# Kernel tuning notes

Hardware: AMD Instinct MI355X
Metric: run time of the kernel (lower is better)

The kernel has to match this reference:

```python
import jax, jax.numpy as jnp
import numpy as np

N = 200000   # nodes
E = 6400000  # directed edges (avg degree 32)
F = 128      # num_features
C = 16       # num_classes
H1, H2, H3 = 4, 4, 2  # hardcoded GCN hidden dims from the source


def setup_inputs():
    key = jax.random.key(0)
    ks = jax.random.split(key, 10)
    x = jax.random.normal(ks[0], (N, F), dtype=jnp.float32)
    edge_index = jax.random.randint(ks[1], (2, E), 0, N, dtype=jnp.int32)
    def lin(k, fin, fout):
        return jax.random.normal(k, (fin, fout), dtype=jnp.float32) / np.sqrt(fin).astype(np.float32)
    return {
        "x": x,
        "W1": lin(ks[2], F, H1),  "b1": jnp.zeros((H1,), jnp.float32),
        "W2": lin(ks[3], H1, H2), "b2": jnp.zeros((H2,), jnp.float32),
        "W3": lin(ks[4], H2, H3), "b3": jnp.zeros((H3,), jnp.float32),
        "Wc": lin(ks[5], H3, C),  "bc": jnp.zeros((C,), jnp.float32),
        "edge_index": edge_index,
    }


def _gcn_conv(h, W, b, src, dst, norm, n):
    # PyG GCNConv: linear first, then normalized scatter-add aggregation, then bias
    h = h @ W                                   # [n, fout]
    msg = h[src] * norm[:, None]                # gather + per-edge scale
    out = jax.ops.segment_sum(msg, dst, num_segments=n)
    return out + b


def reference(x, W1, b1, W2, b2, W3, b3, Wc, bc, edge_index):
    n = x.shape[0]
    # add self-loops (GCNConv default add_self_loops=True)
    loop = jnp.arange(n, dtype=edge_index.dtype)
    src = jnp.concatenate([edge_index[0], loop])
    dst = jnp.concatenate([edge_index[1], loop])
    # symmetric degree normalization: norm_e = deg(dst)^-1/2 * deg(src)^-1/2
    deg = jax.ops.segment_sum(jnp.ones(src.shape[0], dtype=x.dtype), dst, num_segments=n)
    dinv = jnp.where(deg > 0, jax.lax.rsqrt(deg), jnp.zeros_like(deg))
    norm = dinv[src] * dinv[dst]
    h = jnp.tanh(_gcn_conv(x, W1, b1, src, dst, norm, n))
    h = jnp.tanh(_gcn_conv(h, W2, b2, src, dst, norm, n))
    h = jnp.tanh(_gcn_conv(h, W3, b3, src, dst, norm, n))
    out = h @ Wc + bc
    return (out, h)
```

## Files before the change

kernel.cpp:

```cpp
#include <hip/hip_runtime.h>
#include <math.h>


#define NR 1000
#define RNG 200
#define CAP 8192
#define HB 1024
#define EPT 8
#define EPB (HB * EPT)
#define SCAP 8192
#define Q 8
#define LROWS 32
#define LPAD 133


__global__ void k_initcur(int* __restrict__ cursor) {
    int t = blockIdx.x * blockDim.x + threadIdx.x;
    if (t < NR) cursor[t * 16] = t * CAP;
}

__global__ __launch_bounds__(HB) void k_build(const int* __restrict__ src,
                                              const int* __restrict__ dst,
                                              int* __restrict__ cursor,
                                              int* __restrict__ csrp, int e) {
    __shared__ int hist[NR];
    __shared__ int scn[HB];
    __shared__ int start[NR + 1];
    __shared__ int gbase[NR];
    __shared__ int cur[NR];
    __shared__ int buf[EPB];

    int t = threadIdx.x;
    for (int i = t; i < NR; i += HB) hist[i] = 0;
    __syncthreads();

    int ds[EPT], sr[EPT];
    int base = blockIdx.x * EPB;
#pragma unroll
    for (int k = 0; k < 2; k++) {
        int idx = base + k * HB * 4 + t * 4;
        if (idx + 3 < e) {
            int4 d4 = *(const int4*)(dst + idx);
            int4 s4 = *(const int4*)(src + idx);
            ds[4 * k + 0] = d4.x; ds[4 * k + 1] = d4.y; ds[4 * k + 2] = d4.z; ds[4 * k + 3] = d4.w;
            sr[4 * k + 0] = s4.x; sr[4 * k + 1] = s4.y; sr[4 * k + 2] = s4.z; sr[4 * k + 3] = s4.w;
        } else {
#pragma unroll
            for (int j = 0; j < 4; j++) {
                int i2 = idx + j;
                if (i2 < e) { ds[4 * k + j] = dst[i2]; sr[4 * k + j] = src[i2]; }
                else ds[4 * k + j] = -1;
            }
        }
    }
#pragma unroll
    for (int k = 0; k < EPT; k++)
        if (ds[k] >= 0) atomicAdd(&hist[ds[k] / RNG], 1);
    __syncthreads();

    scn[t] = (t < NR) ? hist[t] : 0;
    __syncthreads();
    for (int off = 1; off < HB; off <<= 1) {
        int add = (t >= off) ? scn[t - off] : 0;
        __syncthreads();
        scn[t] += add;
        __syncthreads();
    }
    if (t < NR) {
        int c = hist[t];
        int st = scn[t] - c;
        start[t] = st;
        cur[t] = st;
        gbase[t] = c ? atomicAdd(&cursor[t * 16], c) : 0;
    }
    if (t == 0) start[NR] = scn[NR - 1];
    __syncthreads();

#pragma unroll
    for (int k = 0; k < EPT; k++) {
        if (ds[k] >= 0) {
            int bin = ds[k] / RNG;
            int p = atomicAdd(&cur[bin], 1);
            buf[p] = (sr[k] << 8) | (ds[k] - bin * RNG);
        }
    }
    __syncthreads();

    int total = start[NR];
    for (int j = t; j < total; j += HB) {
        int lo = 0, hi = NR;
        while (hi - lo > 1) {
            int mid = (lo + hi) >> 1;
            if (start[mid] <= j) lo = mid; else hi = mid;
        }
        int g = gbase[lo] + (j - start[lo]);
        if (g < (lo + 1) * CAP) csrp[g] = buf[j];
    }
}


__global__ __launch_bounds__(1024) void k_sortbin(int* __restrict__ csrp,
                                                  const int* __restrict__ cursor,
                                                  float* __restrict__ dinv, int n) {
    __shared__ int deg[RNG];
    __shared__ int off[RNG];
    __shared__ int cur[RNG];
    __shared__ int sbuf[SCAP];
    int t = threadIdx.x, b = blockIdx.x;
    int s0 = b * CAP;
    int cnt = cursor[b * 16] - s0;
    if (cnt < 0) cnt = 0; if (cnt > CAP) cnt = CAP;

    for (int i = t; i < RNG; i += 1024) deg[i] = 0;
    __syncthreads();
    for (int j = t; j < cnt; j += 1024)
        atomicAdd(&deg[csrp[s0 + j] & 255], 1);
    __syncthreads();

    if (t < RNG) off[t] = deg[t];
    __syncthreads();
    for (int d = 1; d < RNG; d <<= 1) {
        int u = 0;
        if (t < RNG && t >= d) u = off[t - d];
        __syncthreads();
        if (t < RNG) off[t] += u;
        __syncthreads();
    }
    if (t < RNG) cur[t] = off[t] - deg[t];
    __syncthreads();

    for (int j = t; j < cnt; j += 1024) {
        int p = csrp[s0 + j];
        int r = atomicAdd(&cur[p & 255], 1);
        if (r < SCAP) sbuf[r] = p;
    }
    __syncthreads();
    int lim = (cnt < SCAP) ? cnt : SCAP;
    for (int j = t; j < lim; j += 1024)
        csrp[s0 + j] = sbuf[j];

    int basen = b * RNG;
    for (int i = t; i < RNG; i += 1024) {
        int node = basen + i;
        if (node < n) dinv[node] = rsqrtf(1.0f + (float)deg[i]);
    }
}


__global__ __launch_bounds__(256) void k_linear1(const float* __restrict__ x,
                                                 const float* __restrict__ W1,
                                                 const float* __restrict__ dinv,
                                                 float4* __restrict__ g1, int n) {
    __shared__ float xs[LROWS * LPAD];
    int t = threadIdx.x;
    int q = t & 7, r = t >> 3;
    int row0 = blockIdx.x * LROWS;

    float4 w[16];
#pragma unroll
    for (int i = 0; i < 16; i++) w[i] = ((const float4*)W1)[q * 16 + i];

    const float4* xg = (const float4*)(x + (size_t)row0 * 128);
    int maxI = (n - row0) * 32;
#pragma unroll
    for (int k = 0; k < 4; k++) {
        int idx = t + k * 256;
        if (idx < maxI) {
            float4 v = xg[idx];
            int rr = idx >> 5, cc = (idx & 31) << 2;
            *(float4*)&xs[rr * LPAD + cc] = v;
        }
    }
    __syncthreads();

    float p0 = 0.f, p1 = 0.f, p2 = 0.f, p3 = 0.f;
    const float* xr = &xs[r * LPAD + q * 16];
#pragma unroll
    for (int j = 0; j < 4; j++) {
        float4 xv = *(const float4*)(xr + 4 * j);
        float4 wa = w[4 * j + 0], wb = w[4 * j + 1], wc = w[4 * j + 2], wd = w[4 * j + 3];
        p0 += xv.x * wa.x + xv.y * wb.x + xv.z * wc.x + xv.w * wd.x;
        p1 += xv.x * wa.y + xv.y * wb.y + xv.z * wc.y + xv.w * wd.y;
        p2 += xv.x * wa.z + xv.y * wb.z + xv.z * wc.z + xv.w * wd.z;
        p3 += xv.x * wa.w + xv.y * wb.w + xv.z * wc.w + xv.w * wd.w;
    }
#pragma unroll
    for (int off = 1; off < 8; off <<= 1) {
        p0 += __shfl_xor(p0, off, 64);
        p1 += __shfl_xor(p1, off, 64);
        p2 += __shfl_xor(p2, off, 64);
        p3 += __shfl_xor(p3, off, 64);
    }
    int row = row0 + r;
    if (q == 0 && row < n) {
        float dv = dinv[row];
        g1[row] = make_float4(dv * p0, dv * p1, dv * p2, dv * p3);
    }
}


#define PUSH4() { qd[qc * 256 + t] = cd; \
    qv[(qc * 4 + 0) * 256 + t] = a0; qv[(qc * 4 + 1) * 256 + t] = a1; \
    qv[(qc * 4 + 2) * 256 + t] = a2; qv[(qc * 4 + 3) * 256 + t] = a3; qc++; }
#define EDGE4(di, gv) { int d_ = (di) & 255; \
    if (d_ != cd) { if (cd >= 0) PUSH4(); cd = d_; a0 = gv.x; a1 = gv.y; a2 = gv.z; a3 = gv.w; } \
    else { a0 += gv.x; a1 += gv.y; a2 += gv.z; a3 += gv.w; } }
#define FLUSH4() { for (int q = 0; q < Q; q++) { if (q < qc) { int dd = qd[q * 256 + t]; \
    atomicAdd(&acc[dd * 5 + 0], qv[(q * 4 + 0) * 256 + t]); \
    atomicAdd(&acc[dd * 5 + 1], qv[(q * 4 + 1) * 256 + t]); \
    atomicAdd(&acc[dd * 5 + 2], qv[(q * 4 + 2) * 256 + t]); \
    atomicAdd(&acc[dd * 5 + 3], qv[(q * 4 + 3) * 256 + t]); } } qc = 0; }

#define EDGELOOP4P() \
    int s0 = b * CAP; \
    int cnt = cursor[b * 16] - s0; if (cnt < 0) cnt = 0; if (cnt > CAP) cnt = CAP; \
    int per = (((cnt + 255) >> 8) + 3) & ~3; \
    int lo = s0 + t * per; \
    int hi = lo + per; int eE = s0 + cnt; if (hi > eE) hi = eE; \
    int cd = -1; float a0 = 0, a1 = 0, a2 = 0, a3 = 0; \
    int qc = 0; \
    int4 pA, pB; \
    float4 gA0, gA1, gA2, gA3; \
    if (lo < hi) { \
        pA = *(const int4*)(csrp + lo); \
        int mA = hi - lo; \
        int e1 = (mA > 1) ? pA.y : pA.x; \
        int e2 = (mA > 2) ? pA.z : pA.x; \
        int e3 = (mA > 3) ? pA.w : pA.x; \
        gA0 = gin[(unsigned)pA.x >> 8]; gA1 = gin[(unsigned)e1 >> 8]; \
        gA2 = gin[(unsigned)e2 >> 8]; gA3 = gin[(unsigned)e3 >> 8]; \
        int jB = lo + 4; \
        pB = *(const int4*)(csrp + ((jB < hi) ? jB : lo)); \
    } \
    for (int j = lo; j < hi; j += 4) { \
        int4 p = pA; \
        float4 g0 = gA0, g1 = gA1, g2 = gA2, g3 = gA3; \
        int m = hi - j; \
        int jn = j + 4; \
        pA = pB; \
        if (jn < hi) { \
            int mN = hi - jn; \
            int e1 = (mN > 1) ? pA.y : pA.x; \
            int e2 = (mN > 2) ? pA.z : pA.x; \
            int e3 = (mN > 3) ? pA.w : pA.x; \
            gA0 = gin[(unsigned)pA.x >> 8]; gA1 = gin[(unsigned)e1 >> 8]; \
            gA2 = gin[(unsigned)e2 >> 8]; gA3 = gin[(unsigned)e3 >> 8]; \
        } \
        int jB2 = j + 8; \
        pB = *(const int4*)(csrp + ((jB2 < hi) ? jB2 : lo)); \
        int i1 = (m > 1) ? p.y : p.x; \
        int i2 = (m > 2) ? p.z : p.x; \
        int i3 = (m > 3) ? p.w : p.x; \
        EDGE4(p.x, g0); \
        if (m > 1) EDGE4(i1, g1); \
        if (m > 2) EDGE4(i2, g2); \
        if (m > 3) EDGE4(i3, g3); \
        if (__any(qc >= Q - 3)) FLUSH4(); \
    } \
    if (cd >= 0) PUSH4(); \
    FLUSH4(); \
    __syncthreads();

__global__ __launch_bounds__(256) void k_bagg44s(const int* __restrict__ csrp,
                                                 const int* __restrict__ cursor,
                                                 const float* __restrict__ dinv,
                                                 const float4* __restrict__ gin,
                                                 float4* __restrict__ gout,
                                                 const float* __restrict__ W,
                                                 const float* __restrict__ bv, int n) {
    __shared__ float acc[RNG * 5];
    __shared__ float qv[Q * 4 * 256];
    __shared__ int   qd[Q * 256];
    int t = threadIdx.x, b = blockIdx.x;
    for (int i = t; i < RNG * 5; i += 256) acc[i] = 0.0f;
    __syncthreads();
    EDGELOOP4P();
    int basen = b * RNG;
    for (int i = t; i < RNG; i += 256) {
        int node = basen + i;
        if (node >= n) continue;
        float4 gs = gin[node];
        float dv = dinv[node];
        float t0 = tanhf(dv * (gs.x + acc[i * 5 + 0]) + bv[0]);
        float t1 = tanhf(dv * (gs.y + acc[i * 5 + 1]) + bv[1]);
        float t2 = tanhf(dv * (gs.z + acc[i * 5 + 2]) + bv[2]);
        float t3 = tanhf(dv * (gs.w + acc[i * 5 + 3]) + bv[3]);
        float4 o;
        o.x = dv * (t0 * W[0] + t1 * W[4] + t2 * W[8]  + t3 * W[12]);
        o.y = dv * (t0 * W[1] + t1 * W[5] + t2 * W[9]  + t3 * W[13]);
        o.z = dv * (t0 * W[2] + t1 * W[6] + t2 * W[10] + t3 * W[14]);
        o.w = dv * (t0 * W[3] + t1 * W[7] + t2 * W[11] + t3 * W[15]);
        gout[node] = o;
    }
}

__global__ __launch_bounds__(256) void k_bagg42s(const int* __restrict__ csrp,
                                                 const int* __restrict__ cursor,
                                                 const float* __restrict__ dinv,
                                                 const float4* __restrict__ gin,
                                                 float2* __restrict__ gout,
                                                 const float* __restrict__ W,
                                                 const float* __restrict__ bv, int n) {
    __shared__ float acc[RNG * 5];
    __shared__ float qv[Q * 4 * 256];
    __shared__ int   qd[Q * 256];
    int t = threadIdx.x, b = blockIdx.x;
    for (int i = t; i < RNG * 5; i += 256) acc[i] = 0.0f;
    __syncthreads();
    EDGELOOP4P();
    int basen = b * RNG;
    for (int i = t; i < RNG; i += 256) {
        int node = basen + i;
        if (node >= n) continue;
        float4 gs = gin[node];
        float dv = dinv[node];
        float t0 = tanhf(dv * (gs.x + acc[i * 5 + 0]) + bv[0]);
        float t1 = tanhf(dv * (gs.y + acc[i * 5 + 1]) + bv[1]);
        float t2 = tanhf(dv * (gs.z + acc[i * 5 + 2]) + bv[2]);
        float t3 = tanhf(dv * (gs.w + acc[i * 5 + 3]) + bv[3]);
        float h0 = t0 * W[0] + t1 * W[2] + t2 * W[4] + t3 * W[6];
        float h1 = t0 * W[1] + t1 * W[3] + t2 * W[5] + t3 * W[7];
        gout[node] = make_float2(dv * h0, dv * h1);
    }
}

#define PUSH2() { qd[qc * 256 + t] = cd; \
    qv[(qc * 2 + 0) * 256 + t] = a0; qv[(qc * 2 + 1) * 256 + t] = a1; qc++; }
#define EDGE2(di, gv) { int d_ = (di) & 255; \
    if (d_ != cd) { if (cd >= 0) PUSH2(); cd = d_; a0 = gv.x; a1 = gv.y; } \
    else { a0 += gv.x; a1 += gv.y; } }
#define FLUSH2() { for (int q = 0; q < Q; q++) { if (q < qc) { int dd = qd[q * 256 + t]; \
    atomicAdd(&acc[dd * 3 + 0], qv[(q * 2 + 0) * 256 + t]); \
    atomicAdd(&acc[dd * 3 + 1], qv[(q * 2 + 1) * 256 + t]); } } qc = 0; }

__global__ __launch_bounds__(256) void k_bagg2outs(const int* __restrict__ csrp,
                                                   const int* __restrict__ cursor,
                                                   const float* __restrict__ dinv,
                                                   const float2* __restrict__ gin,
                                                   const float* __restrict__ b3,
                                                   const float* __restrict__ Wc,
                                                   const float* __restrict__ bc,
                                                   float* __restrict__ out,
                                                   float2* __restrict__ hout, int n) {
    __shared__ float acc[RNG * 3];
    __shared__ float qv[Q * 2 * 256];
    __shared__ int   qd[Q * 256];
    int t = threadIdx.x, b = blockIdx.x;
    for (int i = t; i < RNG * 3; i += 256) acc[i] = 0.0f;
    __syncthreads();
    int s0 = b * CAP;
    int cnt = cursor[b * 16] - s0; if (cnt < 0) cnt = 0; if (cnt > CAP) cnt = CAP;
    int per = (((cnt + 255) >> 8) + 3) & ~3;
    int lo = s0 + t * per;
    int hi = lo + per; int eE = s0 + cnt; if (hi > eE) hi = eE;
    int cd = -1; float a0 = 0, a1 = 0;
    int qc = 0;
    int4 pA, pB;
    float2 gA0, gA1, gA2, gA3;
    if (lo < hi) {
        pA = *(const int4*)(csrp + lo);
        int mA = hi - lo;
        int e1 = (mA > 1) ? pA.y : pA.x;
        int e2 = (mA > 2) ? pA.z : pA.x;
        int e3 = (mA > 3) ? pA.w : pA.x;
        gA0 = gin[(unsigned)pA.x >> 8]; gA1 = gin[(unsigned)e1 >> 8];
        gA2 = gin[(unsigned)e2 >> 8]; gA3 = gin[(unsigned)e3 >> 8];
        int jB = lo + 4;
        pB = *(const int4*)(csrp + ((jB < hi) ? jB : lo));
    }
    for (int j = lo; j < hi; j += 4) {
        int4 p = pA;
        float2 g0 = gA0, g1 = gA1, g2 = gA2, g3 = gA3;
        int m = hi - j;
        int jn = j + 4;
        pA = pB;
        if (jn < hi) {
            int mN = hi - jn;
            int e1 = (mN > 1) ? pA.y : pA.x;
            int e2 = (mN > 2) ? pA.z : pA.x;
            int e3 = (mN > 3) ? pA.w : pA.x;
            gA0 = gin[(unsigned)pA.x >> 8]; gA1 = gin[(unsigned)e1 >> 8];
            gA2 = gin[(unsigned)e2 >> 8]; gA3 = gin[(unsigned)e3 >> 8];
        }
        int jB2 = j + 8;
        pB = *(const int4*)(csrp + ((jB2 < hi) ? jB2 : lo));
        int i1 = (m > 1) ? p.y : p.x;
        int i2 = (m > 2) ? p.z : p.x;
        int i3 = (m > 3) ? p.w : p.x;
        EDGE2(p.x, g0);
        if (m > 1) EDGE2(i1, g1);
        if (m > 2) EDGE2(i2, g2);
        if (m > 3) EDGE2(i3, g3);
        if (__any(qc >= Q - 3)) FLUSH2();
    }
    if (cd >= 0) PUSH2();
    FLUSH2();
    __syncthreads();
    int basen = b * RNG;
    for (int i = t; i < RNG; i += 256) {
        int node = basen + i;
        if (node >= n) continue;
        float2 gs = gin[node];
        float dv = dinv[node];
        float t0 = tanhf(dv * (gs.x + acc[i * 3 + 0]) + b3[0]);
        float t1 = tanhf(dv * (gs.y + acc[i * 3 + 1]) + b3[1]);
        hout[node] = make_float2(t0, t1);
        float4* o = (float4*)(out + (size_t)node * 16);
#pragma unroll
        for (int q = 0; q < 4; q++) {
            float4 v;
            v.x = t0 * Wc[4 * q + 0] + t1 * Wc[16 + 4 * q + 0] + bc[4 * q + 0];
            v.y = t0 * Wc[4 * q + 1] + t1 * Wc[16 + 4 * q + 1] + bc[4 * q + 1];
            v.z = t0 * Wc[4 * q + 2] + t1 * Wc[16 + 4 * q + 2] + bc[4 * q + 2];
            v.w = t0 * Wc[4 * q + 3] + t1 * Wc[16 + 4 * q + 3] + bc[4 * q + 3];
            o[q] = v;
        }
    }
}


__global__ void k_count(const int* __restrict__ dst, int* __restrict__ cnt, int e) {
    int i = blockIdx.x * blockDim.x + threadIdx.x;
    if (i < e) atomicAdd(&cnt[dst[i]], 1);
}

__global__ void k_dinv_i(const int* __restrict__ cnt, float* __restrict__ dinv, int n) {
    int i = blockIdx.x * blockDim.x + threadIdx.x;
    if (i < n) dinv[i] = rsqrtf(1.0f + (float)cnt[i]);
}

__global__ void f_linear1(const float* __restrict__ x, const float* __restrict__ W1,
                          const float* __restrict__ dinv,
                          float* __restrict__ h, float* __restrict__ agg, int n) {
    int lane = threadIdx.x & 63;
    int wave = blockIdx.x * (blockDim.x >> 6) + (threadIdx.x >> 6);
    int nwaves = gridDim.x * (blockDim.x >> 6);
    float4 w0 = ((const float4*)W1)[2 * lane];
    float4 w1 = ((const float4*)W1)[2 * lane + 1];
    for (int row = wave; row < n; row += nwaves) {
        float2 xv = ((const float2*)(x + (size_t)row * 128))[lane];
        float p0 = xv.x * w0.x + xv.y * w1.x;
        float p1 = xv.x * w0.y + xv.y * w1.y;
        float p2 = xv.x * w0.z + xv.y * w1.z;
        float p3 = xv.x * w0.w + xv.y * w1.w;
#pragma unroll
        for (int off = 32; off; off >>= 1) {
            p0 += __shfl_xor(p0, off, 64);
            p1 += __shfl_xor(p1, off, 64);
            p2 += __shfl_xor(p2, off, 64);
            p3 += __shfl_xor(p3, off, 64);
        }
        if (lane == 0) {
            float dv = dinv[row]; float dv2 = dv * dv;
            ((float4*)h)[row] = make_float4(p0, p1, p2, p3);
            ((float4*)agg)[row] = make_float4(dv2 * p0, dv2 * p1, dv2 * p2, dv2 * p3);
        }
    }
}

__global__ void k_edge4(const int* __restrict__ src, const int* __restrict__ dst,
                        const float* __restrict__ dinv, const float* __restrict__ h,
                        float* __restrict__ agg, int e) {
    int i = blockIdx.x * blockDim.x + threadIdx.x;
    if (i >= e) return;
    int s = src[i], d = dst[i];
    float w = dinv[s] * dinv[d];
    float4 hv = ((const float4*)h)[s];
    float* a = agg + 4 * (size_t)d;
    unsafeAtomicAdd(a + 0, w * hv.x);
    unsafeAtomicAdd(a + 1, w * hv.y);
    unsafeAtomicAdd(a + 2, w * hv.z);
    unsafeAtomicAdd(a + 3, w * hv.w);
}

__global__ void k_edge2(const int* __restrict__ src, const int* __restrict__ dst,
                        const float* __restrict__ dinv, const float* __restrict__ h,
                        float* __restrict__ agg, int e) {
    int i = blockIdx.x * blockDim.x + threadIdx.x;
    if (i >= e) return;
    int s = src[i], d = dst[i];
    float w = dinv[s] * dinv[d];
    float2 hv = ((const float2*)h)[s];
    float* a = agg + 2 * (size_t)d;
    unsafeAtomicAdd(a + 0, w * hv.x);
    unsafeAtomicAdd(a + 1, w * hv.y);
}

__global__ void k_fin44(float* __restrict__ h, float* __restrict__ agg,
                        const float* __restrict__ dinv,
                        const float* __restrict__ W, const float* __restrict__ b, int n) {
    int i = blockIdx.x * blockDim.x + threadIdx.x;
    if (i >= n) return;
    float4 a = ((const float4*)agg)[i];
    float t0 = tanhf(a.x + b[0]);
    float t1 = tanhf(a.y + b[1]);
    float t2 = tanhf(a.z + b[2]);
    float t3 = tanhf(a.w + b[3]);
    float hn[4];
#pragma unroll
    for (int k = 0; k < 4; k++)
        hn[k] = t0 * W[k] + t1 * W[4 + k] + t2 * W[8 + k] + t3 * W[12 + k];
    float dv = dinv[i], dv2 = dv * dv;
    ((float4*)h)[i] = make_float4(hn[0], hn[1], hn[2], hn[3]);
    ((float4*)agg)[i] = make_float4(dv2 * hn[0], dv2 * hn[1], dv2 * hn[2], dv2 * hn[3]);
}

__global__ void k_fin42(const float* __restrict__ agg, float* __restrict__ h3,
                        float* __restrict__ agg3, const float* __restrict__ dinv,
                        const float* __restrict__ W, const float* __restrict__ b, int n) {
    int i = blockIdx.x * blockDim.x + threadIdx.x;
    if (i >= n) return;
    float4 a = ((const float4*)agg)[i];
    float t0 = tanhf(a.x + b[0]);
    float t1 = tanhf(a.y + b[1]);
    float t2 = tanhf(a.z + b[2]);
    float t3 = tanhf(a.w + b[3]);
    float h0 = t0 * W[0] + t1 * W[2] + t2 * W[4] + t3 * W[6];
    float h1 = t0 * W[1] + t1 * W[3] + t2 * W[5] + t3 * W[7];
    float dv = dinv[i], dv2 = dv * dv;
    ((float2*)h3)[i] = make_float2(h0, h1);
    ((float2*)agg3)[i] = make_float2(dv2 * h0, dv2 * h1);
}

__global__ void k_final_old(const float* __restrict__ agg3,
                            const float* __restrict__ Wc, const float* __restrict__ b3,
                            const float* __restrict__ bc,
                            float* __restrict__ out, float* __restrict__ hout, int n) {
    int i = blockIdx.x * blockDim.x + threadIdx.x;
    if (i >= n) return;
    float2 a = ((const float2*)agg3)[i];
    float t0 = tanhf(a.x + b3[0]);
    float t1 = tanhf(a.y + b3[1]);
    ((float2*)hout)[i] = make_float2(t0, t1);
    float4* o = (float4*)(out + (size_t)i * 16);
#pragma unroll
    for (int q = 0; q < 4; q++) {
        float4 v;
        v.x = t0 * Wc[4 * q + 0] + t1 * Wc[16 + 4 * q + 0] + bc[4 * q + 0];
        v.y = t0 * Wc[4 * q + 1] + t1 * Wc[16 + 4 * q + 1] + bc[4 * q + 1];
        v.z = t0 * Wc[4 * q + 2] + t1 * Wc[16 + 4 * q + 2] + bc[4 * q + 2];
        v.w = t0 * Wc[4 * q + 3] + t1 * Wc[16 + 4 * q + 3] + bc[4 * q + 3];
        o[q] = v;
    }
}


extern "C" void kernel_launch(void* const* d_in, const int* in_sizes, int n_in,
                              void* d_out, int out_size, void* d_ws, size_t ws_size,
                              hipStream_t stream) {
    const float* x   = (const float*)d_in[0];
    const float* W1  = (const float*)d_in[1];
    const float* b1  = (const float*)d_in[2];
    const float* W2  = (const float*)d_in[3];
    const float* b2  = (const float*)d_in[4];
    const float* W3  = (const float*)d_in[5];
    const float* b3  = (const float*)d_in[6];
    const float* Wc  = (const float*)d_in[7];
    const float* bc  = (const float*)d_in[8];
    const int* eidx  = (const int*)d_in[9];

    const int n = in_sizes[0] / 128;
    const int e = in_sizes[9] / 2;
    const int* src = eidx;
    const int* dst = eidx + e;

    float* out_c = (float*)d_out;
    float* out_h = (float*)d_out + 16 * (size_t)n;

    const int B = 256;
    const int gn = (n + B - 1) / B;
    const int ge = (e + B - 1) / B;
    const int nbE = (e + EPB - 1) / EPB;

    size_t nP = ((size_t)n + 3) & ~(size_t)3;

    int* csrp    = (int*)d_ws;
    int* cursor  = csrp + (size_t)NR * CAP + 4096;
    float* dinv  = (float*)(cursor + NR * 16);
    float* g1    = dinv + nP;
    float* g2    = g1 + 4 * nP;
    float* g3    = g2 + 4 * nP;
    size_t need  = (size_t)((char*)(g3 + 2 * nP) - (char*)d_ws);

    bool fast = (ws_size >= need) && (n <= NR * RNG) && (n < (1 << 18));

    if (fast) {
        k_initcur<<<(NR + 255) / 256, 256, 0, stream>>>(cursor);
        k_build<<<nbE, HB, 0, stream>>>(src, dst, cursor, csrp, e);
        k_sortbin<<<NR, 1024, 0, stream>>>(csrp, cursor, dinv, n);

        k_linear1<<<(n + LROWS - 1) / LROWS, 256, 0, stream>>>(x, W1, dinv, (float4*)g1, n);
        k_bagg44s<<<NR, 256, 0, stream>>>(csrp, cursor, dinv, (const float4*)g1,
                                          (float4*)g2, W2, b1, n);
        k_bagg42s<<<NR, 256, 0, stream>>>(csrp, cursor, dinv, (const float4*)g2,
                                          (float2*)g3, W3, b2, n);
        k_bagg2outs<<<NR, 256, 0, stream>>>(csrp, cursor, dinv, (const float2*)g3,
                                            b3, Wc, bc, out_c, (float2*)out_h, n);
    } else {
        int* fcnt   = (int*)d_ws;
        float* fdnv = (float*)d_ws + nP;
        float* h    = fdnv + nP;
        float* agg  = h + 4 * nP;
        float* h3   = agg + 4 * nP;
        float* agg3 = h3 + 2 * nP;

        hipMemsetAsync(fcnt, 0, (size_t)n * sizeof(int), stream);
        k_count<<<ge, B, 0, stream>>>(dst, fcnt, e);
        k_dinv_i<<<gn, B, 0, stream>>>(fcnt, fdnv, n);
        f_linear1<<<(n + 3) / 4, B, 0, stream>>>(x, W1, fdnv, h, agg, n);
        k_edge4<<<ge, B, 0, stream>>>(src, dst, fdnv, h, agg, e);
        k_fin44<<<gn, B, 0, stream>>>(h, agg, fdnv, W2, b1, n);
        k_edge4<<<ge, B, 0, stream>>>(src, dst, fdnv, h, agg, e);
        k_fin42<<<gn, B, 0, stream>>>(agg, h3, agg3, fdnv, W3, b2, n);
        k_edge2<<<ge, B, 0, stream>>>(src, dst, fdnv, h3, agg3, e);
        k_final_old<<<gn, B, 0, stream>>>(agg3, Wc, b3, bc, out_c, (float*)out_h, n);
    }
}
```

Baseline: 422.7 us.

## Use wider bins split into quarter-blocks with padded segments, drop LDS flush queues

The bins become 400 nodes wide (500 bins with larger capacity), and each bin is split into four 100-node quarters. Each quarter's edge segment is padded to a multiple of 4 with dummy entries that point to a zeroed sentinel row, so the aggregation loops can drop their tail masking. The aggregation kernels launch four blocks per bin and accumulate straight into a small LDS array with atomics, replacing the per-thread queue-and-flush buffers. k_build now stores the bin id per edge instead of binary-searching for it. The changes aim to raise occupancy and cut LDS use and branching, at the cost of more LDS atomic contention and larger sort buffers.

Result: faster. 376.3 us (-11.0%).

```diff
diff --git a/kernel.cpp b/kernel.cpp
--- a/kernel.cpp
+++ b/kernel.cpp
@@ -2,22 +2,27 @@
 #include <math.h>
 
 
-#define NR 1000
-#define RNG 200
-#define CAP 8192
+#define NR 500
+#define RNG 400
+#define CAP 16384
 #define HB 1024
 #define EPT 8
 #define EPB (HB * EPT)
-#define SCAP 8192
-#define Q 8
+#define SCAP 14348
+#define QBLK 100
 #define LROWS 32
 #define LPAD 133
 
 
-__global__ void k_initcur(int* __restrict__ cursor) {
+__global__ void k_initcur(int* __restrict__ cursor, float* __restrict__ g1,
+                          float* __restrict__ g2, float* __restrict__ g3, int n) {
     int t = blockIdx.x * blockDim.x + threadIdx.x;
     if (t < NR) cursor[t * 16] = t * CAP;
-}
+    if (t < 4) g1[4 * (size_t)n + t] = 0.0f;
+    if (t >= 4 && t < 8) g2[4 * (size_t)n + (t - 4)] = 0.0f;
+    if (t >= 8 && t < 10) g3[2 * (size_t)n + (t - 8)] = 0.0f;
+}
+
 
 __global__ __launch_bounds__(HB) void k_build(const int* __restrict__ src,
                                               const int* __restrict__ dst,
@@ -29,6 +34,7 @@
     __shared__ int gbase[NR];
     __shared__ int cur[NR];
     __shared__ int buf[EPB];
+    __shared__ short bbin[EPB];
 
     int t = threadIdx.x;
     for (int i = t; i < NR; i += HB) hist[i] = 0;
@@ -81,30 +87,29 @@
         if (ds[k] >= 0) {
             int bin = ds[k] / RNG;
             int p = atomicAdd(&cur[bin], 1);
-            buf[p] = (sr[k] << 8) | (ds[k] - bin * RNG);
+            buf[p] = (sr[k] << 9) | (ds[k] - bin * RNG);
+            bbin[p] = (short)bin;
         }
     }
     __syncthreads();
 
     int total = start[NR];
     for (int j = t; j < total; j += HB) {
-        int lo = 0, hi = NR;
-        while (hi - lo > 1) {
-            int mid = (lo + hi) >> 1;
-            if (start[mid] <= j) lo = mid; else hi = mid;
-        }
-        int g = gbase[lo] + (j - start[lo]);
-        if (g < (lo + 1) * CAP) csrp[g] = buf[j];
+        int bin = bbin[j];
+        int g = gbase[bin] + (j - start[bin]);
+        if (g < (bin + 1) * CAP) csrp[g] = buf[j];
     }
 }
 
 
 __global__ __launch_bounds__(1024) void k_sortbin(int* __restrict__ csrp,
                                                   const int* __restrict__ cursor,
+                                                  int* __restrict__ split,
                                                   float* __restrict__ dinv, int n) {
     __shared__ int deg[RNG];
     __shared__ int off[RNG];
     __shared__ int cur[RNG];
+    __shared__ int qb[5];
     __shared__ int sbuf[SCAP];
     int t = threadIdx.x, b = blockIdx.x;
     int s0 = b * CAP;
@@ -114,7 +119,7 @@
     for (int i = t; i < RNG; i += 1024) deg[i] = 0;
     __syncthreads();
     for (int j = t; j < cnt; j += 1024)
-        atomicAdd(&deg[csrp[s0 + j] & 255], 1);
+        atomicAdd(&deg[csrp[s0 + j] & 511], 1);
     __syncthreads();
 
     if (t < RNG) off[t] = deg[t];
@@ -126,16 +131,45 @@
         if (t < RNG) off[t] += u;
         __syncthreads();
     }
-    if (t < RNG) cur[t] = off[t] - deg[t];
+    __syncthreads();
+
+    if (t == 0) {
+        int e0 = off[99], e1 = off[199], e2 = off[299], e3 = off[399];
+        int b1 = (e0 + 3) & ~3;
+        int b2 = (b1 + (e1 - e0) + 3) & ~3;
+        int b3 = (b2 + (e2 - e1) + 3) & ~3;
+        int b4 = (b3 + (e3 - e2) + 3) & ~3;
+        qb[0] = 0; qb[1] = b1; qb[2] = b2; qb[3] = b3; qb[4] = b4;
+        split[b * 4 + 0] = b1; split[b * 4 + 1] = b2;
+        split[b * 4 + 2] = b3; split[b * 4 + 3] = b4;
+    }
+    __syncthreads();
+
+    if (t < RNG) {
+        int q = t / 100;
+        int bstart = (q == 0) ? 0 : off[q * 100 - 1];
+        cur[t] = (off[t] - deg[t]) - bstart + qb[q];
+    }
     __syncthreads();
 
     for (int j = t; j < cnt; j += 1024) {
         int p = csrp[s0 + j];
-        int r = atomicAdd(&cur[p & 255], 1);
+        int r = atomicAdd(&cur[p & 511], 1);
         if (r < SCAP) sbuf[r] = p;
     }
     __syncthreads();
-    int lim = (cnt < SCAP) ? cnt : SCAP;
+
+    if (t < 12) {
+        int q = t / 3, sl = t - q * 3;
+        int eq = off[q * 100 + 99];
+        int sq = (q == 0) ? 0 : off[q * 100 - 1];
+        int realend = qb[q] + (eq - sq);
+        int pos = realend + sl;
+        if (pos < qb[q + 1] && pos < SCAP) sbuf[pos] = (n << 9) | (q * 100);
+    }
+    __syncthreads();
+
+    int lim = qb[4]; if (lim > SCAP) lim = SCAP;
     for (int j = t; j < lim; j += 1024)
         csrp[s0 + j] = sbuf[j];
 
@@ -199,84 +233,65 @@
 }
 
 
-#define PUSH4() { qd[qc * 256 + t] = cd; \
-    qv[(qc * 4 + 0) * 256 + t] = a0; qv[(qc * 4 + 1) * 256 + t] = a1; \
-    qv[(qc * 4 + 2) * 256 + t] = a2; qv[(qc * 4 + 3) * 256 + t] = a3; qc++; }
-#define EDGE4(di, gv) { int d_ = (di) & 255; \
+#define PUSH4() { atomicAdd(&acc[cd * 5 + 0], a0); atomicAdd(&acc[cd * 5 + 1], a1); \
+    atomicAdd(&acc[cd * 5 + 2], a2); atomicAdd(&acc[cd * 5 + 3], a3); }
+#define EDGE4(di, gv) { int d_ = ((di) & 511) - qoff; \
     if (d_ != cd) { if (cd >= 0) PUSH4(); cd = d_; a0 = gv.x; a1 = gv.y; a2 = gv.z; a3 = gv.w; } \
     else { a0 += gv.x; a1 += gv.y; a2 += gv.z; a3 += gv.w; } }
-#define FLUSH4() { for (int q = 0; q < Q; q++) { if (q < qc) { int dd = qd[q * 256 + t]; \
-    atomicAdd(&acc[dd * 5 + 0], qv[(q * 4 + 0) * 256 + t]); \
-    atomicAdd(&acc[dd * 5 + 1], qv[(q * 4 + 1) * 256 + t]); \
-    atomicAdd(&acc[dd * 5 + 2], qv[(q * 4 + 2) * 256 + t]); \
-    atomicAdd(&acc[dd * 5 + 3], qv[(q * 4 + 3) * 256 + t]); } } qc = 0; }
 
 #define EDGELOOP4P() \
-    int s0 = b * CAP; \
-    int cnt = cursor[b * 16] - s0; if (cnt < 0) cnt = 0; if (cnt > CAP) cnt = CAP; \
-    int per = (((cnt + 255) >> 8) + 3) & ~3; \
-    int lo = s0 + t * per; \
-    int hi = lo + per; int eE = s0 + cnt; if (hi > eE) hi = eE; \
+    int bin = b >> 2, qq = b & 3; \
+    int qoff = qq * 100; \
+    int s0 = bin * CAP; \
+    int lo0 = qq ? split[bin * 4 + qq - 1] : 0; \
+    int hi0 = split[bin * 4 + qq]; \
+    int L = hi0 - lo0; \
+    int per = (((L + 255) >> 8) + 3) & ~3; \
+    int lo = s0 + lo0 + t * per; \
+    int hi = lo + per; int eE = s0 + hi0; if (hi > eE) hi = eE; \
     int cd = -1; float a0 = 0, a1 = 0, a2 = 0, a3 = 0; \
-    int qc = 0; \
     int4 pA, pB; \
     float4 gA0, gA1, gA2, gA3; \
     if (lo < hi) { \
         pA = *(const int4*)(csrp + lo); \
-        int mA = hi - lo; \
-        int e1 = (mA > 1) ? pA.y : pA.x; \
-        int e2 = (mA > 2) ? pA.z : pA.x; \
-        int e3 = (mA > 3) ? pA.w : pA.x; \
-        gA0 = gin[(unsigned)pA.x >> 8]; gA1 = gin[(unsigned)e1 >> 8]; \
-        gA2 = gin[(unsigned)e2 >> 8]; gA3 = gin[(unsigned)e3 >> 8]; \
+        gA0 = gin[(unsigned)pA.x >> 9]; gA1 = gin[(unsigned)pA.y >> 9]; \
+        gA2 = gin[(unsigned)pA.z >> 9]; gA3 = gin[(unsigned)pA.w >> 9]; \
         int jB = lo + 4; \
         pB = *(const int4*)(csrp + ((jB < hi) ? jB : lo)); \
     } \
     for (int j = lo; j < hi; j += 4) { \
         int4 p = pA; \
-        float4 g0 = gA0, g1 = gA1, g2 = gA2, g3 = gA3; \
-        int m = hi - j; \
+        float4 g0 = gA0, g1v = gA1, g2v = gA2, g3v = gA3; \
         int jn = j + 4; \
         pA = pB; \
         if (jn < hi) { \
-            int mN = hi - jn; \
-            int e1 = (mN > 1) ? pA.y : pA.x; \
-            int e2 = (mN > 2) ? pA.z : pA.x; \
-            int e3 = (mN > 3) ? pA.w : pA.x; \
-            gA0 = gin[(unsigned)pA.x >> 8]; gA1 = gin[(unsigned)e1 >> 8]; \
-            gA2 = gin[(unsigned)e2 >> 8]; gA3 = gin[(unsigned)e3 >> 8]; \
+            gA0 = gin[(unsigned)pA.x >> 9]; gA1 = gin[(unsigned)pA.y >> 9]; \
+            gA2 = gin[(unsigned)pA.z >> 9]; gA3 = gin[(unsigned)pA.w >> 9]; \
         } \
         int jB2 = j + 8; \
         pB = *(const int4*)(csrp + ((jB2 < hi) ? jB2 : lo)); \
-        int i1 = (m > 1) ? p.y : p.x; \
-        int i2 = (m > 2) ? p.z : p.x; \
-        int i3 = (m > 3) ? p.w : p.x; \
         EDGE4(p.x, g0); \
-        if (m > 1) EDGE4(i1, g1); \
-        if (m > 2) EDGE4(i2, g2); \
-        if (m > 3) EDGE4(i3, g3); \
-        if (__any(qc >= Q - 3)) FLUSH4(); \
+        EDGE4(p.y, g1v); \
+        EDGE4(p.z, g2v); \
+        EDGE4(p.w, g3v); \
     } \
     if (cd >= 0) PUSH4(); \
-    FLUSH4(); \
     __syncthreads();
 
 __global__ __launch_bounds__(256) void k_bagg44s(const int* __restrict__ csrp,
-                                                 const int* __restrict__ cursor,
+                                                 const int* __restrict__ split,
                                                  const float* __restrict__ dinv,
                                                  const float4* __restrict__ gin,
                                                  float4* __restrict__ gout,
                                                  const float* __restrict__ W,
                                                  const float* __restrict__ bv, int n) {
-    __shared__ float acc[RNG * 5];
-    __shared__ float qv[Q * 4 * 256];
-    __shared__ int   qd[Q * 256];
+    __shared__ float acc[QBLK * 5];
     int t = threadIdx.x, b = blockIdx.x;
-    for (int i = t; i < RNG * 5; i += 256) acc[i] = 0.0f;
+    for (int i = t; i < QBLK * 5; i += 256) acc[i] = 0.0f;
     __syncthreads();
     EDGELOOP4P();
-    int basen = b * RNG;
-    for (int i = t; i < RNG; i += 256) {
+    int basen = (b >> 2) * RNG + qoff;
+    for (int i = t; i < QBLK; i += 256) {
         int node = basen + i;
         if (node >= n) continue;
         float4 gs = gin[node];
@@ -295,21 +310,19 @@
 }
 
 __global__ __launch_bounds__(256) void k_bagg42s(const int* __restrict__ csrp,
-                                                 const int* __restrict__ cursor,
+                                                 const int* __restrict__ split,
                                                  const float* __restrict__ dinv,
                                                  const float4* __restrict__ gin,
                                                  float2* __restrict__ gout,
                                                  const float* __restrict__ W,
                                                  const float* __restrict__ bv, int n) {
-    __shared__ float acc[RNG * 5];
-    __shared__ float qv[Q * 4 * 256];
-    __shared__ int   qd[Q * 256];
+    __shared__ float acc[QBLK * 5];
     int t = threadIdx.x, b = blockIdx.x;
-    for (int i = t; i < RNG * 5; i += 256) acc[i] = 0.0f;
+    for (int i = t; i < QBLK * 5; i += 256) acc[i] = 0.0f;
     __syncthreads();
     EDGELOOP4P();
-    int basen = b * RNG;
-    for (int i = t; i < RNG; i += 256) {
+    int basen = (b >> 2) * RNG + qoff;
+    for (int i = t; i < QBLK; i += 256) {
         int node = basen + i;
         if (node >= n) continue;
         float4 gs = gin[node];
@@ -324,17 +337,13 @@
     }
 }
 
-#define PUSH2() { qd[qc * 256 + t] = cd; \
-    qv[(qc * 2 + 0) * 256 + t] = a0; qv[(qc * 2 + 1) * 256 + t] = a1; qc++; }
-#define EDGE2(di, gv) { int d_ = (di) & 255; \
+#define PUSH2() { atomicAdd(&acc[cd * 3 + 0], a0); atomicAdd(&acc[cd * 3 + 1], a1); }
+#define EDGE2(di, gv) { int d_ = ((di) & 511) - qoff; \
     if (d_ != cd) { if (cd >= 0) PUSH2(); cd = d_; a0 = gv.x; a1 = gv.y; } \
     else { a0 += gv.x; a1 += gv.y; } }
-#define FLUSH2() { for (int q = 0; q < Q; q++) { if (q < qc) { int dd = qd[q * 256 + t]; \
-    atomicAdd(&acc[dd * 3 + 0], qv[(q * 2 + 0) * 256 + t]); \
-    atomicAdd(&acc[dd * 3 + 1], qv[(q * 2 + 1) * 256 + t]); } } qc = 0; }
 
 __global__ __launch_bounds__(256) void k_bagg2outs(const int* __restrict__ csrp,
-                                                   const int* __restrict__ cursor,
+                                                   const int* __restrict__ split,
                                                    const float* __restrict__ dinv,
                                                    const float2* __restrict__ gin,
                                                    const float* __restrict__ b3,
@@ -342,62 +351,49 @@
                                                    const float* __restrict__ bc,
                                                    float* __restrict__ out,
                                                    float2* __restrict__ hout, int n) {
-    __shared__ float acc[RNG * 3];
-    __shared__ float qv[Q * 2 * 256];
-    __shared__ int   qd[Q * 256];
+    __shared__ float acc[QBLK * 3];
     int t = threadIdx.x, b = blockIdx.x;
-    for (int i = t; i < RNG * 3; i += 256) acc[i] = 0.0f;
-    __syncthreads();
-    int s0 = b * CAP;
-    int cnt = cursor[b * 16] - s0; if (cnt < 0) cnt = 0; if (cnt > CAP) cnt = CAP;
-    int per = (((cnt + 255) >> 8) + 3) & ~3;
-    int lo = s0 + t * per;
-    int hi = lo + per; int eE = s0 + cnt; if (hi > eE) hi = eE;
+    for (int i = t; i < QBLK * 3; i += 256) acc[i] = 0.0f;
+    __syncthreads();
+    int bin = b >> 2, qq = b & 3;
+    int qoff = qq * 100;
+    int s0 = bin * CAP;
+    int lo0 = qq ? split[bin * 4 + qq - 1] : 0;
+    int hi0 = split[bin * 4 + qq];
+    int L = hi0 - lo0;
+    int per = (((L + 255) >> 8) + 3) & ~3;
+    int lo = s0 + lo0 + t * per;
+    int hi = lo + per; int eE = s0 + hi0; if (hi > eE) hi = eE;
     int cd = -1; float a0 = 0, a1 = 0;
-    int qc = 0;
     int4 pA, pB;
     float2 gA0, gA1, gA2, gA3;
     if (lo < hi) {
         pA = *(const int4*)(csrp + lo);
-        int mA = hi - lo;
-        int e1 = (mA > 1) ? pA.y : pA.x;
-        int e2 = (mA > 2) ? pA.z : pA.x;
-        int e3 = (mA > 3) ? pA.w : pA.x;
-        gA0 = gin[(unsigned)pA.x >> 8]; gA1 = gin[(unsigned)e1 >> 8];
-        gA2 = gin[(unsigned)e2 >> 8]; gA3 = gin[(unsigned)e3 >> 8];
+        gA0 = gin[(unsigned)pA.x >> 9]; gA1 = gin[(unsigned)pA.y >> 9];
+        gA2 = gin[(unsigned)pA.z >> 9]; gA3 = gin[(unsigned)pA.w >> 9];
         int jB = lo + 4;
         pB = *(const int4*)(csrp + ((jB < hi) ? jB : lo));
     }
     for (int j = lo; j < hi; j += 4) {
         int4 p = pA;
-        float2 g0 = gA0, g1 = gA1, g2 = gA2, g3 = gA3;
-        int m = hi - j;
+        float2 g0 = gA0, g1v = gA1, g2v = gA2, g3v = gA3;
         int jn = j + 4;
         pA = pB;
         if (jn < hi) {
-            int mN = hi - jn;
-            int e1 = (mN > 1) ? pA.y : pA.x;
-            int e2 = (mN > 2) ? pA.z : pA.x;
-            int e3 = (mN > 3) ? pA.w : pA.x;
-            gA0 = gin[(unsigned)pA.x >> 8]; gA1 = gin[(unsigned)e1 >> 8];
-            gA2 = gin[(unsigned)e2 >> 8]; gA3 = gin[(unsigned)e3 >> 8];
+            gA0 = gin[(unsigned)pA.x >> 9]; gA1 = gin[(unsigned)pA.y >> 9];
+            gA2 = gin[(unsigned)pA.z >> 9]; gA3 = gin[(unsigned)pA.w >> 9];
         }
         int jB2 = j + 8;
         pB = *(const int4*)(csrp + ((jB2 < hi) ? jB2 : lo));
-        int i1 = (m > 1) ? p.y : p.x;
-        int i2 = (m > 2) ? p.z : p.x;
-        int i3 = (m > 3) ? p.w : p.x;
         EDGE2(p.x, g0);
-        if (m > 1) EDGE2(i1, g1);
-        if (m > 2) EDGE2(i2, g2);
-        if (m > 3) EDGE2(i3, g3);
-        if (__any(qc >= Q - 3)) FLUSH2();
+        EDGE2(p.y, g1v);
+        EDGE2(p.z, g2v);
+        EDGE2(p.w, g3v);
     }
     if (cd >= 0) PUSH2();
-    FLUSH2();
-    __syncthreads();
-    int basen = b * RNG;
-    for (int i = t; i < RNG; i += 256) {
+    __syncthreads();
+    int basen = bin * RNG + qoff;
+    for (int i = t; i < QBLK; i += 256) {
         int node = basen + i;
         if (node >= n) continue;
         float2 gs = gin[node];
@@ -572,11 +568,12 @@
     const int ge = (e + B - 1) / B;
     const int nbE = (e + EPB - 1) / EPB;
 
-    size_t nP = ((size_t)n + 3) & ~(size_t)3;
+    size_t nP = ((size_t)(n + 4) + 3) & ~(size_t)3;
 
     int* csrp    = (int*)d_ws;
     int* cursor  = csrp + (size_t)NR * CAP + 4096;
-    float* dinv  = (float*)(cursor + NR * 16);
+    int* split   = cursor + NR * 16;
+    float* dinv  = (float*)(split + NR * 4);
     float* g1    = dinv + nP;
     float* g2    = g1 + 4 * nP;
     float* g3    = g2 + 4 * nP;
@@ -585,17 +582,17 @@
     bool fast = (ws_size >= need) && (n <= NR * RNG) && (n < (1 << 18));
 
     if (fast) {
-        k_initcur<<<(NR + 255) / 256, 256, 0, stream>>>(cursor);
+        k_initcur<<<(NR + 255) / 256, 256, 0, stream>>>(cursor, g1, g2, g3, n);
         k_build<<<nbE, HB, 0, stream>>>(src, dst, cursor, csrp, e);
-        k_sortbin<<<NR, 1024, 0, stream>>>(csrp, cursor, dinv, n);
+        k_sortbin<<<NR, 1024, 0, stream>>>(csrp, cursor, split, dinv, n);
 
         k_linear1<<<(n + LROWS - 1) / LROWS, 256, 0, stream>>>(x, W1, dinv, (float4*)g1, n);
-        k_bagg44s<<<NR, 256, 0, stream>>>(csrp, cursor, dinv, (const float4*)g1,
-                                          (float4*)g2, W2, b1, n);
-        k_bagg42s<<<NR, 256, 0, stream>>>(csrp, cursor, dinv, (const float4*)g2,
-                                          (float2*)g3, W3, b2, n);
-        k_bagg2outs<<<NR, 256, 0, stream>>>(csrp, cursor, dinv, (const float2*)g3,
-                                            b3, Wc, bc, out_c, (float2*)out_h, n);
+        k_bagg44s<<<NR * 4, 256, 0, stream>>>(csrp, split, dinv, (const float4*)g1,
+                                              (float4*)g2, W2, b1, n);
+        k_bagg42s<<<NR * 4, 256, 0, stream>>>(csrp, split, dinv, (const float4*)g2,
+                                              (float2*)g3, W3, b2, n);
+        k_bagg2outs<<<NR * 4, 256, 0, stream>>>(csrp, split, dinv, (const float2*)g3,
+                                                b3, Wc, bc, out_c, (float2*)out_h, n);
     } else {
         int* fcnt   = (int*)d_ws;
         float* fdnv = (float*)d_ws + nP;
```
